# Optimization experiments

Hardware: AMD Instinct MI355X
Metric: run time of the kernel (lower is better)

Reference implementation:

```python
import jax, jax.numpy as jnp
import numpy as np

NA, NP, NT = 100000, 200000, 50000      # authors, papers, terms
DA, DP, DT = 128, 128, 64               # input feature dims per node type
E_AP, E_PA, E_TP, E_PT = 400000, 400000, 300000, 300000
H, OUT = 64, 4                          # hidden_channels, out_channels
NEG_SLOPE = 0.01                        # nn.LeakyReLU default


def setup_inputs() -> dict:
    keys = iter(jax.random.split(jax.random.key(0), 64))
    rn = lambda shape, s=0.05: jax.random.normal(next(keys), shape, dtype=jnp.float32) * s
    ri = lambda n, hi: jax.random.randint(next(keys), (n,), 0, hi, dtype=jnp.int32)
    inp = {
        'x_author': rn((NA, DA), 1.0),
        'x_paper': rn((NP, DP), 1.0),
        'x_term': rn((NT, DT), 1.0),
        'src_ap': ri(E_AP, NA), 'dst_ap': ri(E_AP, NP),
        'src_pa': ri(E_PA, NP), 'dst_pa': ri(E_PA, NA),
        'src_tp': ri(E_TP, NT), 'dst_tp': ri(E_TP, NP),
        'src_pt': ri(E_PT, NP), 'dst_pt': ri(E_PT, NT),
    }
    # SAGEConv params per edge type: Wl (on mean-aggregated src feats, with bias),
    # Wr (root/dst feats, no bias) -- matches PyG SAGEConv(lin_l, lin_r).
    dims = {'ap': (DA, DP), 'pa': (DP, DA), 'tp': (DT, DP), 'pt': (DP, DT)}
    for et, (ds, dd) in dims.items():
        inp['l1_' + et + '_Wl'] = rn((ds, H))
        inp['l1_' + et + '_bl'] = rn((H,))
        inp['l1_' + et + '_Wr'] = rn((dd, H))
        inp['l2_' + et + '_Wl'] = rn((H, H))
        inp['l2_' + et + '_bl'] = rn((H,))
        inp['l2_' + et + '_Wr'] = rn((H, H))
    inp['lin_W'] = rn((H, OUT))
    inp['lin_b'] = rn((OUT,))
    return inp


def _sage(x_src, x_dst, src, dst, Wl, bl, Wr):
    """PyG SAGEConv (mean aggr): lin_l(mean_j x_src[j]) + lin_r(x_dst)."""
    n_dst = x_dst.shape[0]
    agg = jax.ops.segment_sum(x_src[src], dst, num_segments=n_dst)        # [n_dst, d_src]
    cnt = jax.ops.segment_sum(jnp.ones_like(dst, dtype=x_src.dtype), dst, num_segments=n_dst)
    mean = agg / jnp.maximum(cnt, 1.0)[:, None]
    return mean @ Wl + bl + x_dst @ Wr


def reference(x_author, x_paper, x_term,
              src_ap, dst_ap, src_pa, dst_pa, src_tp, dst_tp, src_pt, dst_pt,
              l1_ap_Wl, l1_ap_bl, l1_ap_Wr, l1_pa_Wl, l1_pa_bl, l1_pa_Wr,
              l1_tp_Wl, l1_tp_bl, l1_tp_Wr, l1_pt_Wl, l1_pt_bl, l1_pt_Wr,
              l2_ap_Wl, l2_ap_bl, l2_ap_Wr, l2_pa_Wl, l2_pa_bl, l2_pa_Wr,
              l2_tp_Wl, l2_tp_bl, l2_tp_Wr, l2_pt_Wl, l2_pt_bl, l2_pt_Wr,
              lin_W, lin_b):
    lrelu = lambda v: jax.nn.leaky_relu(v, NEG_SLOPE)
    # Layer 1 (HeteroConv, sum across relations into each dst type) + LeakyReLU.
    p1 = lrelu(_sage(x_author, x_paper, src_ap, dst_ap, l1_ap_Wl, l1_ap_bl, l1_ap_Wr)
               + _sage(x_term, x_paper, src_tp, dst_tp, l1_tp_Wl, l1_tp_bl, l1_tp_Wr))
    a1 = lrelu(_sage(x_paper, x_author, src_pa, dst_pa, l1_pa_Wl, l1_pa_bl, l1_pa_Wr))
    # (term output of layer 1 / layer-2 paper & term outputs do not reach the
    # returned 'author' logits -- omitted, exactly as autograd would prune them.)
    # Layer 2: author output only needs paper->author relation.
    a2 = _sage(p1, a1, src_pa, dst_pa, l2_pa_Wl, l2_pa_bl, l2_pa_Wr)
    return a2 @ lin_W + lin_b  # [NA, OUT]
```

## Files before the change

kernel.cpp:

```cpp
#include <hip/hip_runtime.h>

#define NA 100000
#define NP 200000
#define NT 50000
#define E_AP 400000
#define E_PA 400000
#define E_TP 300000
#define E_TOT (E_AP + E_TP + E_PA)
#define HD 64
#define NOUT 4
#define NEG 0.01f
#define M_CNT (2 * NP + NA)
#define SCAN_NB ((M_CNT + 1023) / 1024)

typedef __attribute__((ext_vector_type(8))) short bf16x8;
typedef __attribute__((ext_vector_type(4))) float f32x4;

static __device__ __forceinline__ short f2bf(float f) {
  unsigned u = __float_as_uint(f);
  unsigned r = (u + 0x7FFFu + ((u >> 16) & 1u)) >> 16;
  return (short)r;
}
static __device__ __forceinline__ float bflo(unsigned u) {
  return __uint_as_float(u << 16);
}
static __device__ __forceinline__ float bfhi(unsigned u) {
  return __uint_as_float(u & 0xFFFF0000u);
}

static __device__ __forceinline__ void acc8(float* acc, uint4 u, float w) {
  acc[0] = fmaf(w, bflo(u.x), acc[0]);
  acc[1] = fmaf(w, bfhi(u.x), acc[1]);
  acc[2] = fmaf(w, bflo(u.y), acc[2]);
  acc[3] = fmaf(w, bfhi(u.y), acc[3]);
  acc[4] = fmaf(w, bflo(u.z), acc[4]);
  acc[5] = fmaf(w, bfhi(u.z), acc[5]);
  acc[6] = fmaf(w, bflo(u.w), acc[6]);
  acc[7] = fmaf(w, bfhi(u.w), acc[7]);
}

#define R_NP 16384
#define R_NA 32768
#define R_TP 36864
#define R_BLC 36928
#define R_WFL 37184
#define R_WFR 37440
#define R_BF 37444
#define BZ_NB ((M_CNT / 4 + 255) / 256)
__global__ __launch_bounds__(256) void build_zero_kernel(
    const float* __restrict__ l1_ap_Wl, const float* __restrict__ l1_ap_bl,
    const float* __restrict__ l1_ap_Wr,
    const float* __restrict__ l1_pa_Wl, const float* __restrict__ l1_pa_bl,
    const float* __restrict__ l1_pa_Wr,
    const float* __restrict__ l1_tp_Wl, const float* __restrict__ l1_tp_bl,
    const float* __restrict__ l1_tp_Wr,
    const float* __restrict__ l2_Wl, const float* __restrict__ l2_bl,
    const float* __restrict__ l2_Wr,
    const float* __restrict__ lin_W, const float* __restrict__ lin_b,
    short* __restrict__ Wt_np, short* __restrict__ Wt_na, short* __restrict__ Wt_tp,
    float* __restrict__ blc, float* __restrict__ Wfl, float* __restrict__ Wfr,
    float* __restrict__ bf, int* __restrict__ cnt) {
  int t = blockIdx.x * 256 + threadIdx.x;
  int z4 = t * 4;
  if (z4 < M_CNT) *(int4*)(cnt + z4) = make_int4(0, 0, 0, 0);

  if (t < R_NP) {
    int c = t >> 7, k = t & 127;
    float v = (c < 64) ? l1_pa_Wl[k * 64 + c]
                       : (l1_ap_Wr[k * 64 + (c - 64)] + l1_tp_Wr[k * 64 + (c - 64)]);
    Wt_np[t] = f2bf(v);
  } else if (t < R_NA) {
    int i = t - R_NP;
    int c = i >> 7, k = i & 127;
    float v = (c < 64) ? l1_ap_Wl[k * 64 + c] : l1_pa_Wr[k * 64 + (c - 64)];
    Wt_na[i] = f2bf(v);
  } else if (t < R_TP) {
    int i = t - R_NA;
    int c = i >> 6, k = i & 63;
    Wt_tp[i] = f2bf(l1_tp_Wl[k * 64 + c]);
  } else if (t < R_BLC) {
    int c = t - R_TP;
    blc[c] = l1_ap_bl[c] + l1_tp_bl[c];
  } else if (t < R_WFL) {
    int i = t - R_BLC;
    int k = i >> 2, c = i & 3;
    float s = 0.f;
    for (int j = 0; j < HD; ++j) s += l2_Wl[k * HD + j] * lin_W[j * NOUT + c];
    Wfl[i] = s;
  } else if (t < R_WFR) {
    int i = t - R_WFL;
    int k = i >> 2, c = i & 3;
    float s = 0.f;
    for (int j = 0; j < HD; ++j) s += l2_Wr[k * HD + j] * lin_W[j * NOUT + c];
    Wfr[i] = s;
  } else if (t < R_BF) {
    int c = t - R_WFR;
    float s = lin_b[c];
    for (int j = 0; j < HD; ++j) s += l2_bl[j] * lin_W[j * NOUT + c];
    bf[c] = s;
  }
}

__global__ __launch_bounds__(256) void count_all(const int* __restrict__ dst_ap,
                                                 const int* __restrict__ dst_tp,
                                                 const int* __restrict__ dst_pa,
                                                 int* __restrict__ cnt) {
  int i4 = (blockIdx.x * 256 + threadIdx.x) * 4;
  const int* p;
  int base;
  if (i4 < E_AP) { p = dst_ap + i4; base = 0; }
  else if (i4 < E_AP + E_TP) { p = dst_tp + (i4 - E_AP); base = NP; }
  else if (i4 < E_TOT) { p = dst_pa + (i4 - E_AP - E_TP); base = 2 * NP; }
  else return;
  int4 d = *(const int4*)p;
  atomicAdd(&cnt[base + d.x], 1);
  atomicAdd(&cnt[base + d.y], 1);
  atomicAdd(&cnt[base + d.z], 1);
  atomicAdd(&cnt[base + d.w], 1);
}

__global__ __launch_bounds__(256) void scan1(const int* __restrict__ cnt,
                                             int* __restrict__ offs,
                                             int* __restrict__ bsum) {
  __shared__ int ts[256];
  int t = threadIdx.x;
  int idx = blockIdx.x * 1024 + t * 4;
  int4 v = make_int4(0, 0, 0, 0);
  if (idx < M_CNT) v = *(const int4*)(cnt + idx);
  int s = v.x + v.y + v.z + v.w;
  ts[t] = s;
  __syncthreads();
  for (int off = 1; off < 256; off <<= 1) {
    int a = (t >= off) ? ts[t - off] : 0;
    __syncthreads();
    ts[t] += a;
    __syncthreads();
  }
  int excl = ts[t] - s;
  if (idx < M_CNT) {
    int4 o;
    o.x = excl; o.y = o.x + v.x; o.z = o.y + v.y; o.w = o.z + v.z;
    *(int4*)(offs + idx) = o;
  }
  if (t == 255) bsum[blockIdx.x] = ts[255];
}

__global__ __launch_bounds__(256) void scan2(int* __restrict__ bsum, int nb) {
  __shared__ int ts[256];
  __shared__ int carrysh;
  int t = threadIdx.x;
  int carry = 0;
  for (int base = 0; base < nb; base += 256) {
    int v = (base + t < nb) ? bsum[base + t] : 0;
    ts[t] = v;
    __syncthreads();
    for (int off = 1; off < 256; off <<= 1) {
      int a = (t >= off) ? ts[t - off] : 0;
      __syncthreads();
      ts[t] += a;
      __syncthreads();
    }
    if (base + t < nb) bsum[base + t] = carry + ts[t] - v;
    if (t == 255) carrysh = ts[255];
    __syncthreads();
    carry += carrysh;
    __syncthreads();
  }
}

__global__ __launch_bounds__(256) void scan3(int* __restrict__ offs,
                                             const int* __restrict__ bsum) {
  int add = bsum[blockIdx.x];
  int idx = blockIdx.x * 1024 + threadIdx.x * 4;
  if (idx < M_CNT) {
    int4 v = *(const int4*)(offs + idx);
    v.x += add; v.y += add; v.z += add; v.w += add;
    *(int4*)(offs + idx) = v;
  }
}

__global__ __launch_bounds__(256) void bucket_kernel(
    const int* __restrict__ src_ap, const int* __restrict__ dst_ap,
    const int* __restrict__ src_tp, const int* __restrict__ dst_tp,
    const int* __restrict__ src_pa, const int* __restrict__ dst_pa,
    int* __restrict__ offs, int* __restrict__ ebuf) {
  int i4 = (blockIdx.x * 256 + threadIdx.x) * 4;
  const int *sp, *dp;
  int base;
  if (i4 < E_AP) { sp = src_ap + i4; dp = dst_ap + i4; base = 0; }
  else if (i4 < E_AP + E_TP) { int j = i4 - E_AP; sp = src_tp + j; dp = dst_tp + j; base = NP; }
  else if (i4 < E_TOT) { int j = i4 - E_AP - E_TP; sp = src_pa + j; dp = dst_pa + j; base = 2 * NP; }
  else return;
  int4 s = *(const int4*)sp;
  int4 d = *(const int4*)dp;
  ebuf[atomicAdd(&offs[base + d.x], 1)] = s.x;
  ebuf[atomicAdd(&offs[base + d.y], 1)] = s.y;
  ebuf[atomicAdd(&offs[base + d.z], 1)] = s.z;
  ebuf[atomicAdd(&offs[base + d.w], 1)] = s.w;
}

template <int K, int COLS, bool HAS_OUT1>
static __device__ __forceinline__ void gemm_body(const float* __restrict__ X,
                                                 const short* __restrict__ Wt,
                                                 const float* __restrict__ bias1,
                                                 unsigned short* __restrict__ out0,
                                                 unsigned short* __restrict__ out1,
                                                 int N, int bid) {
  constexpr int NSTEP = K / 32;
  constexpr int NTILE = COLS / 16;
  const int lane = threadIdx.x & 63;
  const int w = threadIdx.x >> 6;
  const int m = lane & 15;
  const int quad = lane >> 4;
  const int rowA = bid * 64 + w * 16 + m;
  const int rl = min(rowA, N - 1);

  bf16x8 afrag[NSTEP];
  const float* xr = X + (size_t)rl * K + quad * 8;
#pragma unroll
  for (int s = 0; s < NSTEP; ++s) {
    float4 v0 = *(const float4*)(xr + s * 32);
    float4 v1 = *(const float4*)(xr + s * 32 + 4);
    bf16x8 a;
    a[0] = f2bf(v0.x); a[1] = f2bf(v0.y); a[2] = f2bf(v0.z); a[3] = f2bf(v0.w);
    a[4] = f2bf(v1.x); a[5] = f2bf(v1.y); a[6] = f2bf(v1.z); a[7] = f2bf(v1.w);
    afrag[s] = a;
  }

  const int orow = bid * 64 + w * 16 + quad * 4;
#pragma unroll
  for (int ct = 0; ct < NTILE; ++ct) {
    f32x4 acc = {0.f, 0.f, 0.f, 0.f};
    const short* wr = Wt + (size_t)(ct * 16 + m) * K + quad * 8;
#pragma unroll
    for (int s = 0; s < NSTEP; ++s) {
      bf16x8 b = *(const bf16x8*)(wr + s * 32);
      acc = __builtin_amdgcn_mfma_f32_16x16x32_bf16(afrag[s], b, acc, 0, 0, 0);
    }
    int col = ct * 16 + m;
    if (HAS_OUT1 && ct >= NTILE / 2) {
      int ocol = col - 64;
      float badd = bias1[ocol];
#pragma unroll
      for (int rg = 0; rg < 4; ++rg) {
        int r = orow + rg;
        if (r < N) out1[(size_t)r * HD + ocol] = (unsigned short)f2bf(acc[rg] + badd);
      }
    } else {
#pragma unroll
      for (int rg = 0; rg < 4; ++rg) {
        int r = orow + rg;
        if (r < N) out0[(size_t)r * HD + col] = (unsigned short)f2bf(acc[rg]);
      }
    }
  }
}

#define GB_P ((NP + 63) / 64)
#define GB_A ((NA + 63) / 64)
#define GB_T ((NT + 63) / 64)

__global__ __launch_bounds__(256) void gemm_all(
    const float* __restrict__ x_paper, const float* __restrict__ x_author,
    const float* __restrict__ x_term,
    const short* __restrict__ Wt_np, const short* __restrict__ Wt_na,
    const short* __restrict__ Wt_tp,
    const float* __restrict__ blc, const float* __restrict__ l1_pa_bl,
    unsigned short* __restrict__ yp, unsigned short* __restrict__ P1root,
    unsigned short* __restrict__ ya, unsigned short* __restrict__ A1root,
    unsigned short* __restrict__ yt) {
  int b = blockIdx.x;
  if (b < GB_P) {
    gemm_body<128, 128, true>(x_paper, Wt_np, blc, yp, P1root, NP, b);
  } else if (b < GB_P + GB_A) {
    gemm_body<128, 128, true>(x_author, Wt_na, l1_pa_bl, ya, A1root, NA, b - GB_P);
  } else {
    gemm_body<64, 64, false>(x_term, Wt_tp, nullptr, yt, nullptr, NT, b - GB_P - GB_A);
  }
}

__global__ __launch_bounds__(256) void paper_agg(
    const unsigned short* __restrict__ ya, const unsigned short* __restrict__ yt,
    const unsigned short* __restrict__ P1root,
    const int* __restrict__ cnt, const int* __restrict__ offs,
    const int* __restrict__ ebuf, const float* __restrict__ Wfl,
    float* __restrict__ z) {
  const int wv = threadIdx.x >> 6;
  const int lane = threadIdx.x & 63;
  const int g = lane >> 3;
  const int l = lane & 7;
  const int p = blockIdx.x * 32 + wv * 8 + g;
  const bool pv = p < NP;
  const int pc = pv ? p : NP - 1;

  const int cA = cnt[pc], cT = cnt[NP + pc];
  const int startA = offs[pc] - cA;
  const int startT = offs[NP + pc] - cT;

  const unsigned short* yab = ya + 8 * l;
  const unsigned short* ytb = yt + 8 * l;

  float accA[8], accT[8];
#pragma unroll
  for (int j = 0; j < 8; ++j) { accA[j] = 0.f; accT[j] = 0.f; }

  const int mx = max(cA, cT);
  for (int i = 0; i < mx; i += 2) {
    const bool a0 = i < cA, a1 = i + 1 < cA;
    const bool t0 = i < cT, t1 = i + 1 < cT;
    int sA0 = ebuf[startA + i];
    int sA1 = ebuf[startA + i + 1];
    int sT0 = ebuf[startT + i];
    int sT1 = ebuf[startT + i + 1];
    sA0 = a0 ? sA0 : 0;
    sA1 = a1 ? sA1 : 0;
    sT0 = t0 ? sT0 : 0;
    sT1 = t1 ? sT1 : 0;
    const uint4 uA0 = *(const uint4*)(yab + (size_t)sA0 * HD);
    const uint4 uA1 = *(const uint4*)(yab + (size_t)sA1 * HD);
    const uint4 uT0 = *(const uint4*)(ytb + (size_t)sT0 * HD);
    const uint4 uT1 = *(const uint4*)(ytb + (size_t)sT1 * HD);
    acc8(accA, uA0, a0 ? 1.f : 0.f);
    acc8(accA, uA1, a1 ? 1.f : 0.f);
    acc8(accT, uT0, t0 ? 1.f : 0.f);
    acc8(accT, uT1, t1 ? 1.f : 0.f);
  }

  const float rA = 1.0f / (float)max(cA, 1);
  const float rT = 1.0f / (float)max(cT, 1);
  uint4 rt = *(const uint4*)(P1root + (size_t)pc * HD + 8 * l);
  float v[8];
  v[0] = bflo(rt.x); v[1] = bfhi(rt.x); v[2] = bflo(rt.y); v[3] = bfhi(rt.y);
  v[4] = bflo(rt.z); v[5] = bfhi(rt.z); v[6] = bflo(rt.w); v[7] = bfhi(rt.w);
  float4 pz = make_float4(0.f, 0.f, 0.f, 0.f);
#pragma unroll
  for (int j = 0; j < 8; ++j) {
    float x = v[j] + accA[j] * rA + accT[j] * rT;
    x = fmaxf(x, NEG * x);
    float4 wf = *(const float4*)(Wfl + (8 * l + j) * 4);
    pz.x += x * wf.x; pz.y += x * wf.y; pz.z += x * wf.z; pz.w += x * wf.w;
  }
#pragma unroll
  for (int m = 1; m < 8; m <<= 1) {
    pz.x += __shfl_xor(pz.x, m);
    pz.y += __shfl_xor(pz.y, m);
    pz.z += __shfl_xor(pz.z, m);
    pz.w += __shfl_xor(pz.w, m);
  }
  if (l == 0 && pv) *(float4*)(z + (size_t)p * NOUT) = pz;
}

__global__ __launch_bounds__(256) void author_agg(
    const unsigned short* __restrict__ yp, const unsigned short* __restrict__ A1root,
    const float* __restrict__ z,
    const int* __restrict__ cnt, const int* __restrict__ offs,
    const int* __restrict__ ebuf, const float* __restrict__ Wfr,
    const float* __restrict__ bf, float* __restrict__ out) {
  const int wv = threadIdx.x >> 6;
  const int lane = threadIdx.x & 63;
  const int g = lane >> 3;
  const int l = lane & 7;
  const int a = blockIdx.x * 32 + wv * 8 + g;
  const bool av = a < NA;
  const int ac = av ? a : NA - 1;

  const int c = cnt[2 * NP + ac];
  const int start = offs[2 * NP + ac] - c;

  const unsigned short* ypb = yp + 8 * l;

  float acc[8];
#pragma unroll
  for (int j = 0; j < 8; ++j) acc[j] = 0.f;
  float4 az = make_float4(0.f, 0.f, 0.f, 0.f);

  for (int i = 0; i < c; i += 2) {
    const bool b1 = i + 1 < c;
    int s0 = ebuf[start + i];
    int s1 = ebuf[min(start + i + 1, E_TOT - 1)];
    s1 = b1 ? s1 : 0;
    const uint4 u0 = *(const uint4*)(ypb + (size_t)s0 * HD);
    const uint4 u1 = *(const uint4*)(ypb + (size_t)s1 * HD);
    const float4 z0 = *(const float4*)(z + (size_t)s0 * NOUT);
    const float4 z1 = *(const float4*)(z + (size_t)s1 * NOUT);
    const float w1 = b1 ? 1.f : 0.f;
    acc8(acc, u0, 1.f);
    acc8(acc, u1, w1);
    az.x = fmaf(w1, z1.x, az.x + z0.x);
    az.y = fmaf(w1, z1.y, az.y + z0.y);
    az.z = fmaf(w1, z1.z, az.z + z0.z);
    az.w = fmaf(w1, z1.w, az.w + z0.w);
  }

  const float r = 1.0f / (float)max(c, 1);
  uint4 rt = *(const uint4*)(A1root + (size_t)ac * HD + 8 * l);
  float v[8];
  v[0] = bflo(rt.x); v[1] = bfhi(rt.x); v[2] = bflo(rt.y); v[3] = bfhi(rt.y);
  v[4] = bflo(rt.z); v[5] = bfhi(rt.z); v[6] = bflo(rt.w); v[7] = bfhi(rt.w);
  float4 o = make_float4(0.f, 0.f, 0.f, 0.f);
#pragma unroll
  for (int j = 0; j < 8; ++j) {
    float x = v[j] + acc[j] * r;
    x = fmaxf(x, NEG * x);
    float4 wf = *(const float4*)(Wfr + (8 * l + j) * 4);
    o.x += x * wf.x; o.y += x * wf.y; o.z += x * wf.z; o.w += x * wf.w;
  }
#pragma unroll
  for (int m = 1; m < 8; m <<= 1) {
    o.x += __shfl_xor(o.x, m);
    o.y += __shfl_xor(o.y, m);
    o.z += __shfl_xor(o.z, m);
    o.w += __shfl_xor(o.w, m);
  }
  if (l == 0 && av) {
    float4 b = *(const float4*)bf;
    o.x += az.x * r + b.x;
    o.y += az.y * r + b.y;
    o.z += az.z * r + b.z;
    o.w += az.w * r + b.w;
    *(float4*)(out + (size_t)a * NOUT) = o;
  }
}

extern "C" void kernel_launch(void* const* d_in, const int* in_sizes, int n_in,
                              void* d_out, int out_size, void* d_ws, size_t ws_size,
                              hipStream_t stream) {
  const float* x_author = (const float*)d_in[0];
  const float* x_paper  = (const float*)d_in[1];
  const float* x_term   = (const float*)d_in[2];
  const int* src_ap = (const int*)d_in[3];
  const int* dst_ap = (const int*)d_in[4];
  const int* src_pa = (const int*)d_in[5];
  const int* dst_pa = (const int*)d_in[6];
  const int* src_tp = (const int*)d_in[7];
  const int* dst_tp = (const int*)d_in[8];
  const float* l1_ap_Wl = (const float*)d_in[11];
  const float* l1_ap_bl = (const float*)d_in[12];
  const float* l1_ap_Wr = (const float*)d_in[13];
  const float* l1_pa_Wl = (const float*)d_in[17];
  const float* l1_pa_bl = (const float*)d_in[18];
  const float* l1_pa_Wr = (const float*)d_in[19];
  const float* l2_pa_Wl = (const float*)d_in[20];
  const float* l2_pa_bl = (const float*)d_in[21];
  const float* l2_pa_Wr = (const float*)d_in[22];
  const float* l1_tp_Wl = (const float*)d_in[23];
  const float* l1_tp_bl = (const float*)d_in[24];
  const float* l1_tp_Wr = (const float*)d_in[25];
  const float* lin_W = (const float*)d_in[35];
  const float* lin_b = (const float*)d_in[36];
  float* out = (float*)d_out;

  char* wsb = (char*)d_ws;
  auto carve = [&](size_t bytes) {
    char* p = wsb;
    wsb += (bytes + 15) & ~(size_t)15;
    return p;
  };
  unsigned short* ya = (unsigned short*)carve((size_t)NA * HD * 2);
  unsigned short* yp = (unsigned short*)carve((size_t)NP * HD * 2);
  unsigned short* yt = (unsigned short*)carve((size_t)NT * HD * 2);
  unsigned short* P1root = (unsigned short*)carve((size_t)NP * HD * 2);
  unsigned short* A1root = (unsigned short*)carve((size_t)NA * HD * 2);
  float* z = (float*)carve((size_t)NP * NOUT * 4);
  int* cnt = (int*)carve((size_t)M_CNT * 4);
  int* offs = (int*)carve((size_t)M_CNT * 4);
  int* bsum = (int*)carve((size_t)SCAN_NB * 4);
  int* ebuf = (int*)carve((size_t)E_TOT * 4);
  short* Wt_np = (short*)carve(128 * 128 * 2);
  short* Wt_na = (short*)carve(128 * 128 * 2);
  short* Wt_tp = (short*)carve(64 * 64 * 2);
  float* blc = (float*)carve(HD * 4);
  float* Wfl = (float*)carve(HD * NOUT * 4);
  float* Wfr = (float*)carve(HD * NOUT * 4);
  float* bf  = (float*)carve(NOUT * 4);

  build_zero_kernel<<<BZ_NB, 256, 0, stream>>>(
      l1_ap_Wl, l1_ap_bl, l1_ap_Wr, l1_pa_Wl, l1_pa_bl, l1_pa_Wr,
      l1_tp_Wl, l1_tp_bl, l1_tp_Wr, l2_pa_Wl, l2_pa_bl, l2_pa_Wr,
      lin_W, lin_b, Wt_np, Wt_na, Wt_tp, blc, Wfl, Wfr, bf, cnt);
  count_all<<<(E_TOT / 4 + 255) / 256, 256, 0, stream>>>(dst_ap, dst_tp, dst_pa, cnt);

  scan1<<<SCAN_NB, 256, 0, stream>>>(cnt, offs, bsum);
  scan2<<<1, 256, 0, stream>>>(bsum, SCAN_NB);
  scan3<<<SCAN_NB, 256, 0, stream>>>(offs, bsum);

  gemm_all<<<GB_P + GB_A + GB_T, 256, 0, stream>>>(
      x_paper, x_author, x_term, Wt_np, Wt_na, Wt_tp, blc, l1_pa_bl,
      yp, P1root, ya, A1root, yt);

  bucket_kernel<<<(E_TOT / 4 + 255) / 256, 256, 0, stream>>>(src_ap, dst_ap, src_tp, dst_tp,
                                                             src_pa, dst_pa, offs, ebuf);

  paper_agg<<<(NP + 31) / 32, 256, 0, stream>>>(ya, yt, P1root, cnt, offs, ebuf, Wfl, z);
  author_agg<<<(NA + 31) / 32, 256, 0, stream>>>(yp, A1root, z, cnt, offs, ebuf, Wfr, bf, out);
}
```

Measured before the change: 523.4 us.

## Stage GEMM weights in swizzled LDS, double rows per block, coalesce output via LDS

The input-projection GEMM now copies the bf16 weight matrix into XOR-swizzled shared memory once per block instead of having every wave read it from global memory. Each block handles 128 rows instead of 64, so each wave computes two 16-row tiles that share every weight fragment. Results are staged through LDS and written back as 16-byte coalesced stores in place of scattered 2-byte stores. In exchange the kernel uses 32 KB of LDS, two extra barriers and more registers for the doubled accumulators, with launch bounds of 4 blocks per SM.

```diff
diff --git a/kernel.cpp b/kernel.cpp
--- a/kernel.cpp
+++ b/kernel.cpp
@@ -205,62 +205,113 @@
                                                  const float* __restrict__ bias1,
                                                  unsigned short* __restrict__ out0,
                                                  unsigned short* __restrict__ out1,
-                                                 int N, int bid) {
+                                                 int N, int bid,
+                                                 unsigned short* __restrict__ lds) {
   constexpr int NSTEP = K / 32;
   constexpr int NTILE = COLS / 16;
-  const int lane = threadIdx.x & 63;
-  const int w = threadIdx.x >> 6;
+  constexpr int WROWB = K * 2;
+  constexpr int WBYTES = COLS * K * 2;
+  const int t = threadIdx.x;
+  const int lane = t & 63;
+  const int w = t >> 6;
   const int m = lane & 15;
   const int quad = lane >> 4;
-  const int rowA = bid * 64 + w * 16 + m;
-  const int rl = min(rowA, N - 1);
-
-  bf16x8 afrag[NSTEP];
-  const float* xr = X + (size_t)rl * K + quad * 8;
-#pragma unroll
-  for (int s = 0; s < NSTEP; ++s) {
-    float4 v0 = *(const float4*)(xr + s * 32);
-    float4 v1 = *(const float4*)(xr + s * 32 + 4);
-    bf16x8 a;
-    a[0] = f2bf(v0.x); a[1] = f2bf(v0.y); a[2] = f2bf(v0.z); a[3] = f2bf(v0.w);
-    a[4] = f2bf(v1.x); a[5] = f2bf(v1.y); a[6] = f2bf(v1.z); a[7] = f2bf(v1.w);
-    afrag[s] = a;
-  }
-
-  const int orow = bid * 64 + w * 16 + quad * 4;
+
+  const int r0 = bid * 128 + w * 16;
+  const int r1 = r0 + 64;
+  bf16x8 a0[NSTEP], a1[NSTEP];
+  {
+    const float* x0 = X + (size_t)min(r0 + m, N - 1) * K + quad * 8;
+    const float* x1 = X + (size_t)min(r1 + m, N - 1) * K + quad * 8;
+#pragma unroll
+    for (int s = 0; s < NSTEP; ++s) {
+      float4 v0 = *(const float4*)(x0 + s * 32);
+      float4 v1 = *(const float4*)(x0 + s * 32 + 4);
+      float4 u0 = *(const float4*)(x1 + s * 32);
+      float4 u1 = *(const float4*)(x1 + s * 32 + 4);
+      bf16x8 a;
+      a[0] = f2bf(v0.x); a[1] = f2bf(v0.y); a[2] = f2bf(v0.z); a[3] = f2bf(v0.w);
+      a[4] = f2bf(v1.x); a[5] = f2bf(v1.y); a[6] = f2bf(v1.z); a[7] = f2bf(v1.w);
+      a0[s] = a;
+      bf16x8 b;
+      b[0] = f2bf(u0.x); b[1] = f2bf(u0.y); b[2] = f2bf(u0.z); b[3] = f2bf(u0.w);
+      b[4] = f2bf(u1.x); b[5] = f2bf(u1.y); b[6] = f2bf(u1.z); b[7] = f2bf(u1.w);
+      a1[s] = b;
+    }
+  }
+
+  {
+    const char* wsrc = (const char*)Wt;
+    char* wdst = (char*)lds;
+#pragma unroll
+    for (int i = 0; i < WBYTES / 4096; ++i) {
+      const int byte = t * 16 + i * 4096;
+      const uint4 v = *(const uint4*)(wsrc + byte);
+      const int row = byte / WROWB;
+      *(uint4*)(wdst + (byte ^ ((row & 7) << 4))) = v;
+    }
+  }
+  __syncthreads();
+
+  f32x4 acc0[NTILE], acc1[NTILE];
 #pragma unroll
   for (int ct = 0; ct < NTILE; ++ct) {
-    f32x4 acc = {0.f, 0.f, 0.f, 0.f};
-    const short* wr = Wt + (size_t)(ct * 16 + m) * K + quad * 8;
+    acc0[ct] = (f32x4){0.f, 0.f, 0.f, 0.f};
+    acc1[ct] = (f32x4){0.f, 0.f, 0.f, 0.f};
+  }
+#pragma unroll
+  for (int ct = 0; ct < NTILE; ++ct) {
+    const int wrow = ct * 16 + m;
+    const int swx = (wrow & 7) << 4;
 #pragma unroll
     for (int s = 0; s < NSTEP; ++s) {
-      bf16x8 b = *(const bf16x8*)(wr + s * 32);
-      acc = __builtin_amdgcn_mfma_f32_16x16x32_bf16(afrag[s], b, acc, 0, 0, 0);
+      const int byte = wrow * WROWB + s * 64 + quad * 16;
+      const bf16x8 b = *(const bf16x8*)((const char*)lds + (byte ^ swx));
+      acc0[ct] = __builtin_amdgcn_mfma_f32_16x16x32_bf16(a0[s], b, acc0[ct], 0, 0, 0);
+      acc1[ct] = __builtin_amdgcn_mfma_f32_16x16x32_bf16(a1[s], b, acc1[ct], 0, 0, 0);
     }
-    int col = ct * 16 + m;
-    if (HAS_OUT1 && ct >= NTILE / 2) {
-      int ocol = col - 64;
-      float badd = bias1[ocol];
-#pragma unroll
-      for (int rg = 0; rg < 4; ++rg) {
-        int r = orow + rg;
-        if (r < N) out1[(size_t)r * HD + ocol] = (unsigned short)f2bf(acc[rg] + badd);
-      }
-    } else {
-#pragma unroll
-      for (int rg = 0; rg < 4; ++rg) {
-        int r = orow + rg;
-        if (r < N) out0[(size_t)r * HD + col] = (unsigned short)f2bf(acc[rg]);
-      }
+  }
+  __syncthreads();
+
+  constexpr int OROWB = COLS * 2;
+#pragma unroll
+  for (int ct = 0; ct < NTILE; ++ct) {
+    const int col = ct * 16 + m;
+    const float add = (HAS_OUT1 && ct >= NTILE / 2) ? bias1[col - 64] : 0.f;
+#pragma unroll
+    for (int rg = 0; rg < 4; ++rg) {
+      const int lr0 = w * 16 + quad * 4 + rg;
+      const int lr1 = lr0 + 64;
+      const int b0 = lr0 * OROWB + col * 2;
+      const int b1 = lr1 * OROWB + col * 2;
+      *(unsigned short*)((char*)lds + (b0 ^ ((lr0 & 7) << 4))) =
+          (unsigned short)f2bf(acc0[ct][rg] + add);
+      *(unsigned short*)((char*)lds + (b1 ^ ((lr1 & 7) << 4))) =
+          (unsigned short)f2bf(acc1[ct][rg] + add);
     }
   }
-}
-
-#define GB_P ((NP + 63) / 64)
-#define GB_A ((NA + 63) / 64)
-#define GB_T ((NT + 63) / 64)
-
-__global__ __launch_bounds__(256) void gemm_all(
+  __syncthreads();
+
+  constexpr int OUTB = 128 * OROWB;
+#pragma unroll
+  for (int i = 0; i < OUTB / 4096; ++i) {
+    const int byte = t * 16 + i * 4096;
+    const int row = byte / OROWB;
+    const int colb = byte - row * OROWB;
+    const uint4 v = *(const uint4*)((const char*)lds + (byte ^ ((row & 7) << 4)));
+    const int grow = bid * 128 + row;
+    if (grow < N) {
+      unsigned short* dst = (HAS_OUT1 && colb >= 128) ? out1 : out0;
+      *(uint4*)((char*)dst + (size_t)grow * (HD * 2) + (colb & 127)) = v;
+    }
+  }
+}
+
+#define GB_P ((NP + 127) / 128)
+#define GB_A ((NA + 127) / 128)
+#define GB_T ((NT + 127) / 128)
+
+__global__ __launch_bounds__(256, 4) void gemm_all(
     const float* __restrict__ x_paper, const float* __restrict__ x_author,
     const float* __restrict__ x_term,
     const short* __restrict__ Wt_np, const short* __restrict__ Wt_na,
@@ -269,13 +320,14 @@
     unsigned short* __restrict__ yp, unsigned short* __restrict__ P1root,
     unsigned short* __restrict__ ya, unsigned short* __restrict__ A1root,
     unsigned short* __restrict__ yt) {
+  __shared__ unsigned short lds[16384];
   int b = blockIdx.x;
   if (b < GB_P) {
-    gemm_body<128, 128, true>(x_paper, Wt_np, blc, yp, P1root, NP, b);
+    gemm_body<128, 128, true>(x_paper, Wt_np, blc, yp, P1root, NP, b, lds);
   } else if (b < GB_P + GB_A) {
-    gemm_body<128, 128, true>(x_author, Wt_na, l1_pa_bl, ya, A1root, NA, b - GB_P);
+    gemm_body<128, 128, true>(x_author, Wt_na, l1_pa_bl, ya, A1root, NA, b - GB_P, lds);
   } else {
-    gemm_body<64, 64, false>(x_term, Wt_tp, nullptr, yt, nullptr, NT, b - GB_P - GB_A);
+    gemm_body<64, 64, false>(x_term, Wt_tp, nullptr, yt, nullptr, NT, b - GB_P - GB_A, lds);
   }
 }
 
```

Result: faster. 469.8 us (-10.2%).
